# Kernel optimization log

Hardware: AMD Instinct MI355X
Metric: run time of the kernel (lower is better)

## Reference

```python
import jax, jax.numpy as jnp
import numpy as np

B = 262144      # points per batch
DIM = 3         # input_dim
L = 16          # levels
T = 19          # log2 hash table size
F = 2           # features per level
N_MIN, N_MAX = 16, 512

_b = np.exp((np.log(N_MAX) - np.log(N_MIN)) / (L - 1))
RES = np.floor(N_MIN * _b ** np.arange(L)).astype(np.float32).reshape(1, 1, L, 1)

# voxel corner offsets [1, DIM, 1, 2^DIM]
_border = np.empty((DIM, 2 ** DIM), dtype=np.uint32)
for i in range(DIM):
    _border[i, :] = np.array(([0] * 2 ** i + [1] * 2 ** i) * 2 ** (DIM - i - 1), dtype=np.uint32)
BORDER = _border.reshape(1, DIM, 1, 2 ** DIM)

# tiny-cuda-nn hash primes; all fit in uint32. Since the torch code takes the
# result mod 2^T (a power of two), int64 and uint32 arithmetic agree on the
# low bits, so uint32 hashing is bit-exact with the original.
PRIMES = np.array([1, 2654435761, 805459861], dtype=np.uint32)
MASK = np.uint32(2 ** T - 1)


def setup_inputs() -> dict:
    key = jax.random.key(0)
    k1, k2 = jax.random.split(key)
    x = jax.random.uniform(k1, (B, DIM), dtype=jnp.float32)  # coords in [0,1)
    tables = jax.random.uniform(k2, (L, 2 ** T, F), dtype=jnp.float32,
                                minval=-1e-4, maxval=1e-4)
    return {"x": x, "tables": tables}


def reference(x, tables):
    res = jnp.asarray(RES)                                   # [1,1,L,1]
    border = jnp.asarray(BORDER)                             # [1,DIM,1,2^DIM]
    primes = jnp.asarray(PRIMES)
    scaled = x[:, :, None, None] * res                       # [B,DIM,L,1]
    grid = jnp.floor(scaled).astype(jnp.uint32) + border     # [B,DIM,L,2^DIM]
    # spatial hash: xor of per-dim coord * prime, mod 2^T
    h = (grid[:, 0] * primes[0]) ^ (grid[:, 1] * primes[1]) ^ (grid[:, 2] * primes[2])
    idx = (h & MASK).astype(jnp.int32)                       # [B,L,2^DIM]
    gathered = tables[jnp.arange(L)[None, :, None], idx]     # [B,L,2^DIM,F]
    # multilinear interpolation weights
    w = jnp.prod(1.0 - jnp.abs(scaled - grid.astype(scaled.dtype)), axis=1)  # [B,L,2^DIM]
    out = jnp.einsum('blv,blvf->blf', w, gathered)           # [B,L,F]
    return out.reshape(x.shape[0], L * F)
```

## Files before the change

### kernel.cpp

```cpp
#include <hip/hip_runtime.h>


#define NB 262144
#define NL 16
#define TSIZE (1u << 19)
#define TMASK ((1u << 19) - 1u)
#define P1 2654435761u
#define P2 805459861u

#define NCL 3
#define LDS_ENT (26 * 26 * 26)
#define CPTS 8192
#define CBLKS (NB / CPTS)
#define CB_PER_XCD ((NCL * CBLKS) / 8)
#define FINE_CHUNKS 256
#define FINE_TOTAL ((NL - NCL) * FINE_CHUNKS)
#define FINE_PER_XCD (FINE_TOTAL / 8)
#define GRID_BLOCKS (8 * (CB_PER_XCD + FINE_PER_XCD))

typedef float vf2 __attribute__((ext_vector_type(2)));
typedef float vf4 __attribute__((ext_vector_type(4)));

__constant__ float RES_C[NL] = {16.f, 20.f, 25.f, 32.f, 40.f, 50.f, 64.f, 80.f,
                                101.f, 128.f, 161.f, 203.f, 256.f, 322.f, 406.f, 512.f};

__device__ __forceinline__ void ngp_point_level(
    float px, float py, float pz, int l, const float* __restrict__ tables,
    float& o0, float& o1) {
  const float res = RES_C[l];
  const float sx = px * res, sy = py * res, sz = pz * res;
  const float fx = floorf(sx), fy = floorf(sy), fz = floorf(sz);
  const unsigned ix = (unsigned)fx, iy = (unsigned)fy, iz = (unsigned)fz;

  const unsigned hy0 = iy * P1, hy1 = hy0 + P1;
  const unsigned hz0 = iz * P2, hz1 = hz0 + P2;

  const float wx0 = 1.0f - fabsf(sx - fx);
  const float wx1 = 1.0f - fabsf(sx - (fx + 1.0f));
  const float wy0 = 1.0f - fabsf(sy - fy);
  const float wy1 = 1.0f - fabsf(sy - (fy + 1.0f));
  const float wz0 = 1.0f - fabsf(sz - fz);
  const float wz1 = 1.0f - fabsf(sz - (fz + 1.0f));

  const vf2* __restrict__ tbl2 = (const vf2*)tables + (size_t)l * TSIZE;
  const vf4* __restrict__ tbl4 = (const vf4*)tables + (size_t)l * (TSIZE / 2);

  unsigned hyz[4];
  hyz[0] = hy0 ^ hz0;
  hyz[1] = hy1 ^ hz0;
  hyz[2] = hy0 ^ hz1;
  hyz[3] = hy1 ^ hz1;

  vf2 g[8];
  if ((ix & 1u) == 0u) {
#pragma unroll
    for (int p = 0; p < 4; ++p) {
      const unsigned i0 = (ix ^ hyz[p]) & TMASK;
      const vf4 q = tbl4[i0 >> 1];
      vf2 lo; lo.x = q.x; lo.y = q.y;
      vf2 hi; hi.x = q.z; hi.y = q.w;
      const bool x0_is_lo = (i0 & 1u) == 0u;
      g[2 * p + 0] = x0_is_lo ? lo : hi;
      g[2 * p + 1] = x0_is_lo ? hi : lo;
    }
  } else {
#pragma unroll
    for (int p = 0; p < 4; ++p) {
      const unsigned i0 = (ix ^ hyz[p]) & TMASK;
      const unsigned i1 = ((ix + 1u) ^ hyz[p]) & TMASK;
      g[2 * p + 0] = tbl2[i0];
      g[2 * p + 1] = tbl2[i1];
    }
  }

  o0 = 0.0f; o1 = 0.0f;
#pragma unroll
  for (int v = 0; v < 8; ++v) {
    const float w = ((v & 1) ? wx1 : wx0) * ((v & 2) ? wy1 : wy0) * ((v & 4) ? wz1 : wz0);
    o0 = fmaf(w, g[v].x, o0);
    o1 = fmaf(w, g[v].y, o1);
  }
}

template <int E>
__device__ __forceinline__ void coarse_block(
    const int lvl, const int cchunk, const float* __restrict__ x,
    const float* __restrict__ tables, vf2* __restrict__ ws,
    vf2* __restrict__ cache) {
  const int tid = threadIdx.x;
  const vf4* __restrict__ tbl4 = (const vf4*)tables + (size_t)lvl * (TSIZE / 2);

  constexpr int HE = (E + 1) / 2;
  constexpr int U = HE * E * E;

  for (int u = tid; u < U; u += 1024) {
    const int iz = u / (HE * E);
    const int rem = u - iz * (HE * E);
    const int iy = rem / HE;
    const int ixh = rem - iy * HE;
    const unsigned ix = 2u * (unsigned)ixh;
    const unsigned h0 = (ix ^ ((unsigned)iy * P1) ^ ((unsigned)iz * P2)) & TMASK;
    const vf4 q = tbl4[h0 >> 1];
    vf2 lo; lo.x = q.x; lo.y = q.y;
    vf2 hi; hi.x = q.z; hi.y = q.w;
    const bool x0_is_lo = (h0 & 1u) == 0u;
    const int d0 = (int)ix + E * (iy + E * iz);
    cache[d0] = x0_is_lo ? lo : hi;
    if ((int)ix + 1 < E) cache[d0 + 1] = x0_is_lo ? hi : lo;
  }
  __syncthreads();

  const float res = RES_C[lvl];
  const int base = cchunk * CPTS;
#pragma unroll
  for (int k = 0; k < CPTS / 1024; ++k) {
    const int b = base + k * 1024 + tid;
    const float px = __builtin_nontemporal_load(x + b * 3 + 0);
    const float py = __builtin_nontemporal_load(x + b * 3 + 1);
    const float pz = __builtin_nontemporal_load(x + b * 3 + 2);

    const float sx = px * res, sy = py * res, sz = pz * res;
    const float fx = floorf(sx), fy = floorf(sy), fz = floorf(sz);
    const int ix = (int)fx, iy = (int)fy, iz = (int)fz;

    const float wx0 = 1.0f - fabsf(sx - fx);
    const float wx1 = 1.0f - fabsf(sx - (fx + 1.0f));
    const float wy0 = 1.0f - fabsf(sy - fy);
    const float wy1 = 1.0f - fabsf(sy - (fy + 1.0f));
    const float wz0 = 1.0f - fabsf(sz - fz);
    const float wz1 = 1.0f - fabsf(sz - (fz + 1.0f));

    const int d = ix + E * (iy + E * iz);
    vf2 g[8];
    g[0] = cache[d];
    g[1] = cache[d + 1];
    g[2] = cache[d + E];
    g[3] = cache[d + E + 1];
    g[4] = cache[d + E * E];
    g[5] = cache[d + E * E + 1];
    g[6] = cache[d + E * E + E];
    g[7] = cache[d + E * E + E + 1];

    float o0 = 0.0f, o1 = 0.0f;
#pragma unroll
    for (int v = 0; v < 8; ++v) {
      const float w = ((v & 1) ? wx1 : wx0) * ((v & 2) ? wy1 : wy0) * ((v & 4) ? wz1 : wz0);
      o0 = fmaf(w, g[v].x, o0);
      o1 = fmaf(w, g[v].y, o1);
    }
    vf2 r; r.x = o0; r.y = o1;
    __builtin_nontemporal_store(r, ws + (size_t)lvl * NB + b);
  }
}

__global__ __launch_bounds__(1024) void ngp_gather_kernel(
    const float* __restrict__ x,
    const float* __restrict__ tables,
    vf2* __restrict__ ws) {
  __shared__ vf2 cache[LDS_ENT];

  const int x8 = blockIdx.x & 7;
  const int j = blockIdx.x >> 3;

  if (j < CB_PER_XCD) {
    const int u = x8 * CB_PER_XCD + j;
    const int lvl = u >> 5;
    const int cchunk = u & 31;
    switch (lvl) {
      case 0: coarse_block<17>(0, cchunk, x, tables, ws, cache); break;
      case 1: coarse_block<21>(1, cchunk, x, tables, ws, cache); break;
      default: coarse_block<26>(2, cchunk, x, tables, ws, cache); break;
    }
    return;
  }

  const int g = x8 * FINE_PER_XCD + (j - CB_PER_XCD);
  const int lvl = NCL + (g >> 8);
  const int b = (g & 255) * 1024 + threadIdx.x;

  const float px = __builtin_nontemporal_load(x + b * 3 + 0);
  const float py = __builtin_nontemporal_load(x + b * 3 + 1);
  const float pz = __builtin_nontemporal_load(x + b * 3 + 2);

  float o0, o1;
  ngp_point_level(px, py, pz, lvl, tables, o0, o1);

  vf2 r; r.x = o0; r.y = o1;
  __builtin_nontemporal_store(r, ws + (size_t)lvl * NB + b);
}

__global__ __launch_bounds__(256) void ngp_transpose_kernel(
    const vf2* __restrict__ ws,
    vf4* __restrict__ out4) {
  __shared__ vf2 tile[NL][257];
  const int t = threadIdx.x;
  const int p0 = blockIdx.x * 256;

#pragma unroll
  for (int l = 0; l < NL; ++l) {
    tile[l][t] = __builtin_nontemporal_load(ws + (size_t)l * NB + p0 + t);
  }
  __syncthreads();

#pragma unroll
  for (int k = 0; k < 8; ++k) {
    const int q = k * 256 + t;
    const int pq = q >> 3;
    const int wq = q & 7;
    const vf2 a = tile[2 * wq + 0][pq];
    const vf2 c = tile[2 * wq + 1][pq];
    vf4 v; v.x = a.x; v.y = a.y; v.z = c.x; v.w = c.y;
    __builtin_nontemporal_store(v, out4 + (size_t)p0 * 8 + q);
  }
}

__global__ __launch_bounds__(256) void ngp_fused_kernel(
    const float* __restrict__ x, const float* __restrict__ tables,
    float* __restrict__ out) {
  const int tid = blockIdx.x * blockDim.x + threadIdx.x;
  const int l = tid & (NL - 1);
  const int b = tid >> 4;
  float o0, o1;
  ngp_point_level(x[b * 3], x[b * 3 + 1], x[b * 3 + 2], l, tables, o0, o1);
  float2 r = make_float2(o0, o1);
  ((float2*)out)[tid] = r;
}

extern "C" void kernel_launch(void* const* d_in, const int* in_sizes, int n_in,
                              void* d_out, int out_size, void* d_ws, size_t ws_size,
                              hipStream_t stream) {
  const float* x = (const float*)d_in[0];
  const float* tables = (const float*)d_in[1];
  float* out = (float*)d_out;

  const size_t ws_needed = (size_t)NL * NB * sizeof(vf2);
  if (ws_size >= ws_needed) {
    vf2* ws = (vf2*)d_ws;
    ngp_gather_kernel<<<GRID_BLOCKS, 1024, 0, stream>>>(x, tables, ws);
    ngp_transpose_kernel<<<NB / 256, 256, 0, stream>>>(ws, (vf4*)out);
  } else {
    ngp_fused_kernel<<<NB * NL / 256, 256, 0, stream>>>(x, tables, out);
  }
}
```

Baseline: 190.7 us.

## Split level-2 LDS cache into z-halves to shrink shared memory footprint

Level 2's coarse cache (26^3 entries) is split into two z-half blocks of 14 planes each, so every block's LDS allocation drops to 26*26*14 vf2. Each half-block loads half the grid but still reads all points in its chunk and processes only those in its z range. This lets more 1024-thread blocks stay resident per CU (launch bounds now request 8 waves per EU) and simplifies the block-to-XCD mapping, so the coarse blocks no longer follow the XCD interleave. In exchange, level-2 coordinates are read twice and there is some divergence from the active-point predicate.

```diff
diff --git a/kernel.cpp b/kernel.cpp
--- a/kernel.cpp
+++ b/kernel.cpp
@@ -9,14 +9,14 @@
 #define P2 805459861u
 
 #define NCL 3
-#define LDS_ENT (26 * 26 * 26)
 #define CPTS 8192
 #define CBLKS (NB / CPTS)
-#define CB_PER_XCD ((NCL * CBLKS) / 8)
+#define COARSE_BLOCKS 128
+#define CLDS_ENT (26 * 26 * 14)
 #define FINE_CHUNKS 256
 #define FINE_TOTAL ((NL - NCL) * FINE_CHUNKS)
 #define FINE_PER_XCD (FINE_TOTAL / 8)
-#define GRID_BLOCKS (8 * (CB_PER_XCD + FINE_PER_XCD))
+#define GRID_BLOCKS (COARSE_BLOCKS + FINE_TOTAL)
 
 typedef float vf2 __attribute__((ext_vector_type(2)));
 typedef float vf4 __attribute__((ext_vector_type(4)));
@@ -83,7 +83,7 @@
 }
 
 template <int E>
-__device__ __forceinline__ void coarse_block(
+__device__ __forceinline__ void coarse_full(
     const int lvl, const int cchunk, const float* __restrict__ x,
     const float* __restrict__ tables, vf2* __restrict__ ws,
     vf2* __restrict__ cache) {
@@ -153,28 +153,104 @@
   }
 }
 
-__global__ __launch_bounds__(1024) void ngp_gather_kernel(
+__device__ __forceinline__ void coarse_half_l2(
+    const int half, const int cchunk, const float* __restrict__ x,
+    const float* __restrict__ tables, vf2* __restrict__ ws,
+    vf2* __restrict__ cache) {
+  const int tid = threadIdx.x;
+  const vf4* __restrict__ tbl4 = (const vf4*)tables + (size_t)2 * (TSIZE / 2);
+
+  const int zb = half ? 13 : 0;
+  const int planes = half ? 13 : 14;
+  const int U = 13 * 26 * planes;
+
+  for (int u = tid; u < U; u += 1024) {
+    const int zp = u / (13 * 26);
+    const int rem = u - zp * (13 * 26);
+    const int iy = rem / 13;
+    const int ixh = rem - iy * 13;
+    const unsigned ix = 2u * (unsigned)ixh;
+    const unsigned iz = (unsigned)(zb + zp);
+    const unsigned h0 = (ix ^ ((unsigned)iy * P1) ^ (iz * P2)) & TMASK;
+    const vf4 q = tbl4[h0 >> 1];
+    vf2 lo; lo.x = q.x; lo.y = q.y;
+    vf2 hi; hi.x = q.z; hi.y = q.w;
+    const bool x0_is_lo = (h0 & 1u) == 0u;
+    const int d0 = (int)ix + 26 * iy + 676 * zp;
+    cache[d0] = x0_is_lo ? lo : hi;
+    if ((int)ix + 1 < 26) cache[d0 + 1] = x0_is_lo ? hi : lo;
+  }
+  __syncthreads();
+
+  const float res = RES_C[2];
+  const int base = cchunk * CPTS;
+#pragma unroll
+  for (int k = 0; k < CPTS / 1024; ++k) {
+    const int b = base + k * 1024 + tid;
+    const float px = __builtin_nontemporal_load(x + b * 3 + 0);
+    const float py = __builtin_nontemporal_load(x + b * 3 + 1);
+    const float pz = __builtin_nontemporal_load(x + b * 3 + 2);
+
+    const float sx = px * res, sy = py * res, sz = pz * res;
+    const float fx = floorf(sx), fy = floorf(sy), fz = floorf(sz);
+    const int ix = (int)fx, iy = (int)fy, iz = (int)fz;
+
+    const bool active = half ? (iz >= 13) : (iz <= 12);
+    if (active) {
+      const float wx0 = 1.0f - fabsf(sx - fx);
+      const float wx1 = 1.0f - fabsf(sx - (fx + 1.0f));
+      const float wy0 = 1.0f - fabsf(sy - fy);
+      const float wy1 = 1.0f - fabsf(sy - (fy + 1.0f));
+      const float wz0 = 1.0f - fabsf(sz - fz);
+      const float wz1 = 1.0f - fabsf(sz - (fz + 1.0f));
+
+      const int d = ix + 26 * iy + 676 * (iz - zb);
+      vf2 g[8];
+      g[0] = cache[d];
+      g[1] = cache[d + 1];
+      g[2] = cache[d + 26];
+      g[3] = cache[d + 27];
+      g[4] = cache[d + 676];
+      g[5] = cache[d + 677];
+      g[6] = cache[d + 702];
+      g[7] = cache[d + 703];
+
+      float o0 = 0.0f, o1 = 0.0f;
+#pragma unroll
+      for (int v = 0; v < 8; ++v) {
+        const float w = ((v & 1) ? wx1 : wx0) * ((v & 2) ? wy1 : wy0) * ((v & 4) ? wz1 : wz0);
+        o0 = fmaf(w, g[v].x, o0);
+        o1 = fmaf(w, g[v].y, o1);
+      }
+      vf2 r; r.x = o0; r.y = o1;
+      __builtin_nontemporal_store(r, ws + (size_t)2 * NB + b);
+    }
+  }
+}
+
+__global__ __launch_bounds__(1024, 8) void ngp_gather2(
     const float* __restrict__ x,
     const float* __restrict__ tables,
     vf2* __restrict__ ws) {
-  __shared__ vf2 cache[LDS_ENT];
-
-  const int x8 = blockIdx.x & 7;
-  const int j = blockIdx.x >> 3;
-
-  if (j < CB_PER_XCD) {
-    const int u = x8 * CB_PER_XCD + j;
-    const int lvl = u >> 5;
-    const int cchunk = u & 31;
-    switch (lvl) {
-      case 0: coarse_block<17>(0, cchunk, x, tables, ws, cache); break;
-      case 1: coarse_block<21>(1, cchunk, x, tables, ws, cache); break;
-      default: coarse_block<26>(2, cchunk, x, tables, ws, cache); break;
+  __shared__ vf2 cache[CLDS_ENT];
+
+  const int bid = blockIdx.x;
+  if (bid < COARSE_BLOCKS) {
+    if (bid < 32) {
+      coarse_full<17>(0, bid & 31, x, tables, ws, cache);
+    } else if (bid < 64) {
+      coarse_full<21>(1, bid & 31, x, tables, ws, cache);
+    } else {
+      const int u = bid - 64;
+      coarse_half_l2(u >> 5, u & 31, x, tables, ws, cache);
     }
     return;
   }
 
-  const int g = x8 * FINE_PER_XCD + (j - CB_PER_XCD);
+  const int fid = bid - COARSE_BLOCKS;
+  const int x8 = fid & 7;
+  const int j = fid >> 3;
+  const int g = x8 * FINE_PER_XCD + j;
   const int lvl = NCL + (g >> 8);
   const int b = (g & 255) * 1024 + threadIdx.x;
 
@@ -236,7 +312,7 @@
   const size_t ws_needed = (size_t)NL * NB * sizeof(vf2);
   if (ws_size >= ws_needed) {
     vf2* ws = (vf2*)d_ws;
-    ngp_gather_kernel<<<GRID_BLOCKS, 1024, 0, stream>>>(x, tables, ws);
+    ngp_gather2<<<GRID_BLOCKS, 1024, 0, stream>>>(x, tables, ws);
     ngp_transpose_kernel<<<NB / 256, 256, 0, stream>>>(ws, (vf4*)out);
   } else {
     ngp_fused_kernel<<<NB * NL / 256, 256, 0, stream>>>(x, tables, out);
```

Measured after the change: 190.8 us. About the same (+0.1%).

## Split coarse-level LDS caches into z-slabs to shrink shared memory and raise occupancy

Applied to the files above, without the earlier changes.

The coarse levels' dense LDS tables are split along z into slabs that fit a 17^3-entry buffer: level 1 becomes two slabs and level 2 five. Each slab block scans its whole point chunk and handles only the points whose cell falls in its z range. The point is that the old 140KB static LDS array, shared by every block of the kernel including the fine hash-gather blocks, allowed only one 1024-thread block per CU. Blocks drop to 512 threads with launch bounds that ask for more resident blocks. The costs are repeated x reads and divergent work in the coarse slab blocks, and coarse blocks no longer use the XCD interleave mapping.

```diff
diff --git a/kernel.cpp b/kernel.cpp
--- a/kernel.cpp
+++ b/kernel.cpp
@@ -9,14 +9,13 @@
 #define P2 805459861u
 
 #define NCL 3
-#define LDS_ENT (26 * 26 * 26)
 #define CPTS 8192
-#define CBLKS (NB / CPTS)
-#define CB_PER_XCD ((NCL * CBLKS) / 8)
-#define FINE_CHUNKS 256
+#define COARSE_BLOCKS 256
+#define CLDS_ENT (17 * 17 * 17)
+#define FINE_CHUNKS 512
 #define FINE_TOTAL ((NL - NCL) * FINE_CHUNKS)
 #define FINE_PER_XCD (FINE_TOTAL / 8)
-#define GRID_BLOCKS (8 * (CB_PER_XCD + FINE_PER_XCD))
+#define GRID_BLOCKS (COARSE_BLOCKS + FINE_TOTAL)
 
 typedef float vf2 __attribute__((ext_vector_type(2)));
 typedef float vf4 __attribute__((ext_vector_type(4)));
@@ -82,29 +81,31 @@
   }
 }
 
-template <int E>
-__device__ __forceinline__ void coarse_block(
-    const int lvl, const int cchunk, const float* __restrict__ x,
+template <int E, int PLANES>
+__device__ __forceinline__ void coarse_slab(
+    const int lvl, const int zbase, const int c_lo, const int c_hi,
+    const int cchunk, const float* __restrict__ x,
     const float* __restrict__ tables, vf2* __restrict__ ws,
     vf2* __restrict__ cache) {
   const int tid = threadIdx.x;
   const vf4* __restrict__ tbl4 = (const vf4*)tables + (size_t)lvl * (TSIZE / 2);
 
   constexpr int HE = (E + 1) / 2;
-  constexpr int U = HE * E * E;
-
-  for (int u = tid; u < U; u += 1024) {
-    const int iz = u / (HE * E);
-    const int rem = u - iz * (HE * E);
+  constexpr int U = HE * E * PLANES;
+
+  for (int u = tid; u < U; u += 512) {
+    const int zp = u / (HE * E);
+    const int rem = u - zp * (HE * E);
     const int iy = rem / HE;
     const int ixh = rem - iy * HE;
     const unsigned ix = 2u * (unsigned)ixh;
-    const unsigned h0 = (ix ^ ((unsigned)iy * P1) ^ ((unsigned)iz * P2)) & TMASK;
+    const unsigned iz = (unsigned)(zbase + zp);
+    const unsigned h0 = (ix ^ ((unsigned)iy * P1) ^ (iz * P2)) & TMASK;
     const vf4 q = tbl4[h0 >> 1];
     vf2 lo; lo.x = q.x; lo.y = q.y;
     vf2 hi; hi.x = q.z; hi.y = q.w;
     const bool x0_is_lo = (h0 & 1u) == 0u;
-    const int d0 = (int)ix + E * (iy + E * iz);
+    const int d0 = (int)ix + E * iy + E * E * zp;
     cache[d0] = x0_is_lo ? lo : hi;
     if ((int)ix + 1 < E) cache[d0 + 1] = x0_is_lo ? hi : lo;
   }
@@ -113,70 +114,78 @@
   const float res = RES_C[lvl];
   const int base = cchunk * CPTS;
 #pragma unroll
-  for (int k = 0; k < CPTS / 1024; ++k) {
-    const int b = base + k * 1024 + tid;
-    const float px = __builtin_nontemporal_load(x + b * 3 + 0);
-    const float py = __builtin_nontemporal_load(x + b * 3 + 1);
-    const float pz = __builtin_nontemporal_load(x + b * 3 + 2);
+  for (int k = 0; k < CPTS / 512; ++k) {
+    const int b = base + k * 512 + tid;
+    const float px = x[b * 3 + 0];
+    const float py = x[b * 3 + 1];
+    const float pz = x[b * 3 + 2];
 
     const float sx = px * res, sy = py * res, sz = pz * res;
     const float fx = floorf(sx), fy = floorf(sy), fz = floorf(sz);
     const int ix = (int)fx, iy = (int)fy, iz = (int)fz;
 
-    const float wx0 = 1.0f - fabsf(sx - fx);
-    const float wx1 = 1.0f - fabsf(sx - (fx + 1.0f));
-    const float wy0 = 1.0f - fabsf(sy - fy);
-    const float wy1 = 1.0f - fabsf(sy - (fy + 1.0f));
-    const float wz0 = 1.0f - fabsf(sz - fz);
-    const float wz1 = 1.0f - fabsf(sz - (fz + 1.0f));
-
-    const int d = ix + E * (iy + E * iz);
-    vf2 g[8];
-    g[0] = cache[d];
-    g[1] = cache[d + 1];
-    g[2] = cache[d + E];
-    g[3] = cache[d + E + 1];
-    g[4] = cache[d + E * E];
-    g[5] = cache[d + E * E + 1];
-    g[6] = cache[d + E * E + E];
-    g[7] = cache[d + E * E + E + 1];
-
-    float o0 = 0.0f, o1 = 0.0f;
-#pragma unroll
-    for (int v = 0; v < 8; ++v) {
-      const float w = ((v & 1) ? wx1 : wx0) * ((v & 2) ? wy1 : wy0) * ((v & 4) ? wz1 : wz0);
-      o0 = fmaf(w, g[v].x, o0);
-      o1 = fmaf(w, g[v].y, o1);
-    }
-    vf2 r; r.x = o0; r.y = o1;
-    __builtin_nontemporal_store(r, ws + (size_t)lvl * NB + b);
-  }
-}
-
-__global__ __launch_bounds__(1024) void ngp_gather_kernel(
+    if (iz >= c_lo && iz <= c_hi) {
+      const float wx0 = 1.0f - fabsf(sx - fx);
+      const float wx1 = 1.0f - fabsf(sx - (fx + 1.0f));
+      const float wy0 = 1.0f - fabsf(sy - fy);
+      const float wy1 = 1.0f - fabsf(sy - (fy + 1.0f));
+      const float wz0 = 1.0f - fabsf(sz - fz);
+      const float wz1 = 1.0f - fabsf(sz - (fz + 1.0f));
+
+      const int d = ix + E * iy + E * E * (iz - zbase);
+      vf2 g[8];
+      g[0] = cache[d];
+      g[1] = cache[d + 1];
+      g[2] = cache[d + E];
+      g[3] = cache[d + E + 1];
+      g[4] = cache[d + E * E];
+      g[5] = cache[d + E * E + 1];
+      g[6] = cache[d + E * E + E];
+      g[7] = cache[d + E * E + E + 1];
+
+      float o0 = 0.0f, o1 = 0.0f;
+#pragma unroll
+      for (int v = 0; v < 8; ++v) {
+        const float w = ((v & 1) ? wx1 : wx0) * ((v & 2) ? wy1 : wy0) * ((v & 4) ? wz1 : wz0);
+        o0 = fmaf(w, g[v].x, o0);
+        o1 = fmaf(w, g[v].y, o1);
+      }
+      vf2 r; r.x = o0; r.y = o1;
+      __builtin_nontemporal_store(r, ws + (size_t)lvl * NB + b);
+    }
+  }
+}
+
+__global__ __launch_bounds__(512, 8) void ngp_gather3(
     const float* __restrict__ x,
     const float* __restrict__ tables,
     vf2* __restrict__ ws) {
-  __shared__ vf2 cache[LDS_ENT];
-
-  const int x8 = blockIdx.x & 7;
-  const int j = blockIdx.x >> 3;
-
-  if (j < CB_PER_XCD) {
-    const int u = x8 * CB_PER_XCD + j;
-    const int lvl = u >> 5;
-    const int cchunk = u & 31;
-    switch (lvl) {
-      case 0: coarse_block<17>(0, cchunk, x, tables, ws, cache); break;
-      case 1: coarse_block<21>(1, cchunk, x, tables, ws, cache); break;
-      default: coarse_block<26>(2, cchunk, x, tables, ws, cache); break;
+  __shared__ vf2 cache[CLDS_ENT];
+
+  const int bid = blockIdx.x;
+  if (bid < COARSE_BLOCKS) {
+    if (bid < 32) {
+      coarse_slab<17, 17>(0, 0, 0, 15, bid, x, tables, ws, cache);
+    } else if (bid < 96) {
+      const int u = bid - 32;
+      const int half = u >> 5;
+      coarse_slab<21, 11>(1, half * 10, half * 10, half * 10 + 9, u & 31,
+                          x, tables, ws, cache);
+    } else {
+      const int u = bid - 96;
+      const int s = u >> 5;
+      coarse_slab<26, 6>(2, 5 * s, 5 * s, 5 * s + 4, u & 31,
+                         x, tables, ws, cache);
     }
     return;
   }
 
-  const int g = x8 * FINE_PER_XCD + (j - CB_PER_XCD);
-  const int lvl = NCL + (g >> 8);
-  const int b = (g & 255) * 1024 + threadIdx.x;
+  const int fid = bid - COARSE_BLOCKS;
+  const int x8 = fid & 7;
+  const int j = fid >> 3;
+  const int g = x8 * FINE_PER_XCD + j;
+  const int lvl = NCL + (g >> 9);
+  const int b = (g & 511) * 512 + threadIdx.x;
 
   const float px = __builtin_nontemporal_load(x + b * 3 + 0);
   const float py = __builtin_nontemporal_load(x + b * 3 + 1);
@@ -236,7 +245,7 @@
   const size_t ws_needed = (size_t)NL * NB * sizeof(vf2);
   if (ws_size >= ws_needed) {
     vf2* ws = (vf2*)d_ws;
-    ngp_gather_kernel<<<GRID_BLOCKS, 1024, 0, stream>>>(x, tables, ws);
+    ngp_gather3<<<GRID_BLOCKS, 512, 0, stream>>>(x, tables, ws);
     ngp_transpose_kernel<<<NB / 256, 256, 0, stream>>>(ws, (vf4*)out);
   } else {
     ngp_fused_kernel<<<NB * NL / 256, 256, 0, stream>>>(x, tables, out);
```

Measured after the change: 190.2 us. No clear change (-0.2%).
